# Kernel tuning notes

Hardware: AMD Instinct MI355X
Metric: run time of the kernel (lower is better)

The kernel has to match this reference:

```python
import jax, jax.numpy as jnp
import numpy as np
import math

B, S, D = 8, 1024, 1024
NH, NKV, HD = 16, 8, 64
BLK_NUM, BLK_SIZE = 128, 8

def apply_rope(x, cos, sin):
    # x: (B,S,H,HD); cos/sin: (S, HD//2)
    x1 = x[..., 0::2]
    x2 = x[..., 1::2]
    c = cos[None, :, None, :]
    s = sin[None, :, None, :]
    r1 = x1 * c - x2 * s
    r2 = x1 * s + x2 * c
    out = jnp.stack([r1, r2], axis=-1).reshape(x.shape)
    return out

def setup_inputs() -> dict:
    key = jax.random.key(0)
    ks = jax.random.split(key, 7)
    x = jax.random.normal(ks[0], (B, S, D), dtype=jnp.float32)
    scale = 1.0 / math.sqrt(D)
    wq = jax.random.normal(ks[1], (D, NH * HD), dtype=jnp.float32) * scale
    wk = jax.random.normal(ks[2], (D, NKV * HD), dtype=jnp.float32) * scale
    wv = jax.random.normal(ks[3], (D, NKV * HD), dtype=jnp.float32) * scale
    wo = jax.random.normal(ks[4], (NH * HD, D), dtype=jnp.float32) * scale
    pos = jnp.arange(S, dtype=jnp.float32)
    inv_freq = 1.0 / (10000.0 ** (jnp.arange(0, HD, 2, dtype=jnp.float32) / HD))
    ang = pos[:, None] * inv_freq[None, :]
    freqs_cis_cos = jnp.cos(ang)
    freqs_cis_sin = jnp.sin(ang)
    return {"x": x, "wq": wq, "wk": wk, "wv": wv, "wo": wo,
            "freqs_cis_cos": freqs_cis_cos, "freqs_cis_sin": freqs_cis_sin,
            "start_pos": 0}

def reference(x, wq, wk, wv, wo, freqs_cis_cos, freqs_cis_sin, start_pos):
    q = (x @ wq).reshape(B, S, NH, HD)
    k = (x @ wk).reshape(B, S, NKV, HD)
    v = (x @ wv).reshape(B, S, NKV, HD)
    q = apply_rope(q, freqs_cis_cos, freqs_cis_sin)
    k = apply_rope(k, freqs_cis_cos, freqs_cis_sin)
    # GQA: repeat kv heads
    rep = NH // NKV
    k = jnp.repeat(k, rep, axis=2)  # (B,S,NH,HD)
    v = jnp.repeat(v, rep, axis=2)
    # block-causal mask: q in block i attends to kv blocks j <= i
    blk_id = jnp.arange(S) // BLK_SIZE
    mask = blk_id[:, None] >= blk_id[None, :]  # (S,S)
    scores = jnp.einsum('bqhd,bkhd->bhqk', q, k) / math.sqrt(HD)
    scores = jnp.where(mask[None, None], scores, -jnp.inf)
    attn = jax.nn.softmax(scores, axis=-1)
    out = jnp.einsum('bhqk,bkhd->bqhd', attn, v).reshape(B, S, NH * HD)
    return out @ wo
```

## Files before the change

### kernel.cpp

```cpp
#include <hip/hip_runtime.h>
#include <cstdint>
#include <math.h>

#define B_   8
#define S_   1024
#define D_   1024
#define NH_  16
#define NKV_ 8
#define HD_  64
#define M_   (B_*S_)

using bf16   = __bf16;
using bf16x4 = __attribute__((ext_vector_type(4))) __bf16;
using bf16x8 = __attribute__((ext_vector_type(8))) __bf16;
using f32x4  = __attribute__((ext_vector_type(4))) float;

__device__ __forceinline__ void gll16(const bf16* g, const bf16* l) {
    __builtin_amdgcn_global_load_lds(
        (const __attribute__((address_space(1))) unsigned int*)(uintptr_t)g,
        (__attribute__((address_space(3))) unsigned int*)(uintptr_t)l,
        16, 0, 0);
}

__device__ __forceinline__ void dsr128(bf16x8& d, const bf16* p) {
    asm volatile("ds_read_b128 %0, %1" : "=v"(d) : "v"((unsigned)(uintptr_t)p));
}
__device__ __forceinline__ void lgkm0() {
    asm volatile("s_waitcnt lgkmcnt(0)" ::: "memory");
    __builtin_amdgcn_sched_barrier(0);
}
__device__ __forceinline__ void vm_wait0()  { asm volatile("s_waitcnt vmcnt(0)"  ::: "memory"); }
__device__ __forceinline__ void vm_wait4()  { asm volatile("s_waitcnt vmcnt(4)"  ::: "memory"); }
__device__ __forceinline__ void vm_wait5()  { asm volatile("s_waitcnt vmcnt(5)"  ::: "memory"); }
__device__ __forceinline__ void vm_wait6()  { asm volatile("s_waitcnt vmcnt(6)"  ::: "memory"); }
__device__ __forceinline__ void bar()       { __builtin_amdgcn_s_barrier(); asm volatile("" ::: "memory"); }

__global__ void k_prep1(const float* __restrict__ x,
                        const float* __restrict__ wq, const float* __restrict__ wk,
                        const float* __restrict__ wv, const float* __restrict__ wo,
                        bf16* __restrict__ xb, bf16* __restrict__ wqkvT, bf16* __restrict__ woT) {
    __shared__ float tile[64 * 65];
    int bid = blockIdx.x;
    int t = threadIdx.x;
    if (bid < 8192) {
        int i = bid * 256 + t;
        float4 v = ((const float4*)x)[i];
        bf16x4 o = { (bf16)v.x, (bf16)v.y, (bf16)v.z, (bf16)v.w };
        ((bf16x4*)xb)[i] = o;
        return;
    }
    int b2 = bid - 8192;
    int bx = b2 % 48, by = b2 / 48;
    const int R = 1024;
    const float* in; bf16* out; int C, xo;
    if (bx < 16)      { in = wq; out = wqkvT;               C = 1024; xo = bx; }
    else if (bx < 24) { in = wk; out = wqkvT + 1024 * 1024; C = 512;  xo = bx - 16; }
    else if (bx < 32) { in = wv; out = wqkvT + 1536 * 1024; C = 512;  xo = bx - 24; }
    else              { in = wo; out = woT;                 C = 1024; xo = bx - 32; }
    int r0 = by * 64, c0 = xo * 64;
    #pragma unroll
    for (int it = 0; it < 16; ++it) {
        int idx = it * 256 + t;
        int r = idx >> 6, c = idx & 63;
        tile[r * 65 + c] = in[(size_t)(r0 + r) * C + c0 + c];
    }
    __syncthreads();
    #pragma unroll
    for (int it = 0; it < 16; ++it) {
        int idx = it * 256 + t;
        int c = idx >> 6, r = idx & 63;
        out[(size_t)(c0 + c) * R + r0 + r] = (bf16)tile[r * 65 + c];
    }
}

template <typename OutT, int NI>
__global__ __launch_bounds__(512, 2) void k_gemm8p(const bf16* __restrict__ A,
                                                   const bf16* __restrict__ Bt,
                                                   OutT* __restrict__ C, int M, int N, int K) {
    constexpr int BN = NI * 64;
    __shared__ __align__(16) bf16 aL2[2 * 256 * 64];
    __shared__ __align__(16) bf16 bL2[2 * BN * 64];
    const int t    = threadIdx.x;
    const int lane = t & 63;
    const int w    = t >> 6;
    const int quad = lane >> 4;
    const int l16  = lane & 15;
    const int wr   = w >> 2;
    const int wc   = w & 3;

    int bid = blockIdx.y * gridDim.x + blockIdx.x;
    int cpx = (gridDim.x * gridDim.y) >> 3;
    int sw  = (bid & 7) * cpx + (bid >> 3);
    int bx  = sw % gridDim.x, by = sw / gridDim.x;
    const int m0 = by * 256;
    const int n0 = bx * BN;

    f32x4 acc[8][NI] = {};

    auto stageA2 = [&](int kb, int dbuf, int itX, int itY) {
        const int k0 = kb << 6;
        #pragma unroll
        for (int u = 0; u < 2; ++u) {
            int it = u ? itY : itX;
            int ci = it * 512 + t;
            int r = ci >> 3, c = ci & 7;
            int cg = c ^ (r & 7);
            gll16(A + (size_t)(m0 + r) * K + k0 + cg * 8, aL2 + dbuf * (256 * 64) + ci * 8);
        }
    };
    auto stageBh = [&](int kb, int dbuf, int nh) {
        const int k0 = kb << 6;
        #pragma unroll
        for (int j = 0; j < NI / 2; ++j) {
            int it = nh * (NI / 2) + j;
            int ci = it * 512 + t;
            int lr = ci >> 3, cs = ci & 7;
            int cg = cs ^ (lr & 7);
            int idx = lr - nh * (BN / 2);
            int wcc = idx / (NI * 8);
            int off = idx % (NI * 8);
            int g   = wcc * (NI * 16) + nh * (NI * 8) + off;
            gll16(Bt + (size_t)(n0 + g) * K + k0 + cg * 8, bL2 + dbuf * (BN * 64) + ci * 8);
        }
    };

    auto loadA = [&](const bf16* aL, int mh, bf16x8 (&af)[8]) {
        #pragma unroll
        for (int mi = 0; mi < 4; ++mi)
            #pragma unroll
            for (int kk = 0; kk < 2; ++kk) {
                int row = wr * 128 + (mh * 4 + mi) * 16 + l16;
                int ch  = (kk * 4 + quad) ^ (row & 7);
                dsr128(af[mi * 2 + kk], &aL[row * 64 + ch * 8]);
            }
    };
    auto loadB = [&](const bf16* bL, int nh, bf16x8 (&bfr)[NI]) {
        #pragma unroll
        for (int j = 0; j < NI / 2; ++j)
            #pragma unroll
            for (int kk = 0; kk < 2; ++kk) {
                int lr = nh * (BN / 2) + wc * (NI * 8) + j * 16 + l16;
                int ch = (kk * 4 + quad) ^ (lr & 7);
                dsr128(bfr[j * 2 + kk], &bL[lr * 64 + ch * 8]);
            }
    };
    auto mmac = [&](int mh, int nh, bf16x8 (&af)[8], bf16x8 (&bfr)[NI]) {
        __builtin_amdgcn_s_setprio(1);
        #pragma unroll
        for (int mi = 0; mi < 4; ++mi)
            #pragma unroll
            for (int j = 0; j < NI / 2; ++j)
                #pragma unroll
                for (int kk = 0; kk < 2; ++kk)
                    acc[mh * 4 + mi][nh * (NI / 2) + j] =
                        __builtin_amdgcn_mfma_f32_16x16x32_bf16(af[mi * 2 + kk], bfr[j * 2 + kk],
                                                                acc[mh * 4 + mi][nh * (NI / 2) + j], 0, 0, 0);
        __builtin_amdgcn_s_setprio(0);
    };

    const int NT = K >> 6;

    auto tile = [&](int T, int bufc) {
        const bf16* aL = aL2 + bufc * (256 * 64);
        const bf16* bL = bL2 + bufc * (BN * 64);
        bf16x8 af[8], bfr[NI];
        loadA(aL, 0, af); loadB(bL, 0, bfr);
        if (T + 1 < NT) stageBh(T + 1, bufc ^ 1, 1);
        bar(); lgkm0();
        mmac(0, 0, af, bfr);
        bar();
        loadB(bL, 1, bfr);
        if (T + 2 < NT) stageA2(T + 2, bufc, 0, 2);
        bar(); lgkm0();
        mmac(0, 1, af, bfr);
        bar();
        loadA(aL, 1, af); loadB(bL, 0, bfr);
        bar(); lgkm0();
        mmac(1, 0, af, bfr);
        bar();
        loadB(bL, 1, bfr);
        if (T + 2 < NT) { stageA2(T + 2, bufc, 1, 3); stageBh(T + 2, bufc, 0); }
        bar(); lgkm0();
        mmac(1, 1, af, bfr);
        if (T + 2 < NT) { if constexpr (NI == 4) vm_wait6(); else vm_wait5(); }
        else vm_wait0();
        bar();
    };

    stageA2(0, 0, 0, 2); stageA2(0, 0, 1, 3); stageBh(0, 0, 0); stageBh(0, 0, 1);
    stageA2(1, 1, 0, 2); stageA2(1, 1, 1, 3); stageBh(1, 1, 0);
    if constexpr (NI == 4) vm_wait6(); else vm_wait5();
    bar();

    for (int T = 0; T < NT; T += 2) {
        tile(T, 0);
        tile(T + 1, 1);
    }

    #pragma unroll
    for (int mi = 0; mi < 8; ++mi)
        #pragma unroll
        for (int ni = 0; ni < NI; ++ni)
            #pragma unroll
            for (int r = 0; r < 4; ++r) {
                int row = m0 + wr * 128 + mi * 16 + quad * 4 + r;
                int col = n0 + wc * (NI * 16) + ni * 16 + l16;
                C[(size_t)row * N + col] = (OutT)acc[mi][ni][r];
            }
}

__global__ void k_prep2(const bf16* __restrict__ qkv, const float* __restrict__ cosg,
                        const float* __restrict__ sing, bf16* __restrict__ qd,
                        bf16* __restrict__ kd, bf16* __restrict__ vt) {
    __shared__ __align__(16) bf16 tile[64 * 72];
    int bid = blockIdx.x;
    int t = threadIdx.x;
    if (bid < 8192) {
        if (t < 192) {
            int token = bid;
            int b = token >> 10, s = token & 1023;
            int hh = t >> 3, i8 = t & 7;
            float4 c4 = *(const float4*)&cosg[s * 32 + i8 * 4];
            float4 s4 = *(const float4*)&sing[s * 32 + i8 * 4];
            int srcBase, dstBase;
            bf16* dst;
            float sf;
            if (hh < 16) {
                srcBase = token * 2048 + hh * 64;
                dstBase = ((b * NH_ + hh) * S_ + s) * 64;
                dst = qd;
                sf = 0.180336879f;
            } else {
                int h = hh - 16;
                srcBase = token * 2048 + 1024 + h * 64;
                dstBase = ((b * NKV_ + h) * S_ + s) * 64;
                dst = kd;
                sf = 1.0f;
            }
            bf16x8 v = *(const bf16x8*)&qkv[srcBase + i8 * 8];
            const float cc[4] = { c4.x, c4.y, c4.z, c4.w };
            const float ss[4] = { s4.x, s4.y, s4.z, s4.w };
            bf16x8 o;
            #pragma unroll
            for (int j = 0; j < 4; ++j) {
                float e  = (float)v[2 * j];
                float od = (float)v[2 * j + 1];
                o[2 * j]     = (bf16)(sf * (e * cc[j] - od * ss[j]));
                o[2 * j + 1] = (bf16)(sf * (e * ss[j] + od * cc[j]));
            }
            *(bf16x8*)&dst[dstBase + i8 * 8] = o;
        }
        return;
    }
    int b2 = bid - 8192;
    int st = b2 & 15;
    int h  = (b2 >> 4) & 7;
    int b  = b2 >> 7;
    int s0 = st * 64;
    #pragma unroll
    for (int it = 0; it < 2; ++it) {
        int ci = it * 256 + t;
        int r = ci >> 3, c = ci & 7;
        *(uint4*)&tile[r * 72 + c * 8] =
            *(const uint4*)&qkv[(size_t)(b * S_ + s0 + r) * 2048 + 1536 + h * 64 + c * 8];
    }
    __syncthreads();
    #pragma unroll
    for (int it = 0; it < 2; ++it) {
        int ci = it * 256 + t;
        int d = ci >> 3, sc = ci & 7;
        int g = sc >> 2, q4 = sc & 3;
        bf16x8 v;
        #pragma unroll
        for (int j = 0; j < 8; ++j) {
            int s_ext = g * 32 + q4 * 4 + (j & 3) + 16 * (j >> 2);
            v[j] = tile[s_ext * 72 + d];
        }
        *(bf16x8*)&vt[(size_t)((b * NKV_ + h) * 64 + d) * S_ + s0 + sc * 8] = v;
    }
}

__global__ __launch_bounds__(256, 4) void k_attn(const bf16* __restrict__ q, const bf16* __restrict__ k,
                                                 const bf16* __restrict__ vt, bf16* __restrict__ out) {
    __shared__ __align__(16) bf16 kt[2 * 64 * 64];
    __shared__ __align__(16) bf16 vtt[2 * 64 * 64];
    int bid = blockIdx.x;
    int qt = 15 - (bid >> 7);
    int combo = bid & 127;
    int b = combo >> 4, h = combo & 15;
    int hkv = h >> 1;
    int t = threadIdx.x;
    int w = t >> 6, lane = t & 63, quad = lane >> 4, l16 = lane & 15;

    const bf16* qh = q + (size_t)(b * NH_ + h) * S_ * 64;
    int qw = qt * 64 + w * 16;
    const bf16* qb = qh + (size_t)(qw + l16) * 64;
    bf16x8 qf0 = *(const bf16x8*)(qb + quad * 8);
    bf16x8 qf1 = *(const bf16x8*)(qb + 32 + quad * 8);

    const bf16* kg = k  + (size_t)(b * NKV_ + hkv) * S_ * 64;
    const bf16* vg = vt + (size_t)(b * NKV_ + hkv) * 64 * S_;

    const int sr0 = t >> 3;
    const int cs  = t & 7;

    auto stage = [&](int u, int buf) {
        int k0 = u * 64;
        #pragma unroll
        for (int it = 0; it < 2; ++it) {
            int r  = sr0 + it * 32;
            int cg = cs ^ (r & 7);
            int ci = it * 256 + t;
            gll16(kg + (size_t)(k0 + r) * 64 + cg * 8, kt  + buf * 4096 + ci * 8);
            gll16(vg + (size_t)r * S_ + k0 + cg * 8,   vtt + buf * 4096 + ci * 8);
        }
    };

    const bf16 one = (bf16)1.0f;
    const bf16x8 vones = { one, one, one, one, one, one, one, one };

    f32x4 o[4] = {};
    f32x4 ol = {};
    const int klim = ((qw + l16) & ~7) + 8;

    auto unit = [&](const bf16* ktb, const bf16* vtb, int k0, bool diag) {
        bf16x8 af[8];
        #pragma unroll
        for (int kk = 0; kk < 2; ++kk)
            #pragma unroll
            for (int f = 0; f < 4; ++f) {
                int row = f * 16 + l16;
                int ch  = (kk * 4 + quad) ^ (row & 7);
                dsr128(af[kk * 4 + f], &ktb[row * 64 + ch * 8]);
            }
        lgkm0();
        f32x4 sc[4] = {};
        __builtin_amdgcn_s_setprio(1);
        #pragma unroll
        for (int kk = 0; kk < 2; ++kk)
            #pragma unroll
            for (int f = 0; f < 4; ++f)
                sc[f] = __builtin_amdgcn_mfma_f32_16x16x32_bf16(af[kk * 4 + f], kk ? qf1 : qf0, sc[f], 0, 0, 0);
        __builtin_amdgcn_s_setprio(0);

        bf16x8 vbf[8];
        #pragma unroll
        for (int dc = 0; dc < 4; ++dc)
            #pragma unroll
            for (int kk = 0; kk < 2; ++kk) {
                int row = dc * 16 + l16;
                int ch  = (kk * 4 + quad) ^ (row & 7);
                dsr128(vbf[dc * 2 + kk], &vtb[row * 64 + ch * 8]);
            }

        float p[4][4];
        #pragma unroll
        for (int f = 0; f < 4; ++f)
            #pragma unroll
            for (int r = 0; r < 4; ++r) {
                float pv = __builtin_amdgcn_exp2f(sc[f][r]);
                if (diag && (k0 + f * 16 + quad * 4 + r >= klim)) pv = 0.f;
                p[f][r] = pv;
            }
        bf16x8 pa0, pa1;
        #pragma unroll
        for (int j = 0; j < 4; ++j) {
            pa0[j]     = (bf16)p[0][j];
            pa0[j + 4] = (bf16)p[1][j];
            pa1[j]     = (bf16)p[2][j];
            pa1[j + 4] = (bf16)p[3][j];
        }
        ol = __builtin_amdgcn_mfma_f32_16x16x32_bf16(pa0, vones, ol, 0, 0, 0);
        ol = __builtin_amdgcn_mfma_f32_16x16x32_bf16(pa1, vones, ol, 0, 0, 0);

        lgkm0();
        __builtin_amdgcn_s_setprio(1);
        #pragma unroll
        for (int dc = 0; dc < 4; ++dc)
            #pragma unroll
            for (int kk = 0; kk < 2; ++kk)
                o[dc] = __builtin_amdgcn_mfma_f32_16x16x32_bf16(kk ? pa1 : pa0, vbf[dc * 2 + kk], o[dc], 0, 0, 0);
        __builtin_amdgcn_s_setprio(0);
    };

    const int NU = qt + 1;
    stage(0, 0);
    asm volatile("" :: "v"(qf0), "v"(qf1));

    int u = 0;
    for (; u + 2 <= NU; u += 2) {
        bar();
        stage(u + 1, 1);
        vm_wait4();
        bar();
        unit(kt, vtt, u * 64, false);
        bar();
        bool hn = (u + 2 < NU);
        if (hn) { stage(u + 2, 0); vm_wait4(); } else vm_wait0();
        bar();
        unit(kt + 4096, vtt + 4096, (u + 1) * 64, (u + 1) == NU - 1);
    }
    if (u < NU) {
        bar();
        vm_wait0();
        bar();
        unit(kt, vtt, u * 64, true);
    }

    #pragma unroll
    for (int r = 0; r < 4; ++r) {
        float invl = 1.0f / ol[r];
        #pragma unroll
        for (int dc = 0; dc < 4; ++dc) {
            int row = qw + quad * 4 + r;
            int col = h * 64 + dc * 16 + l16;
            out[(size_t)(b * S_ + row) * 1024 + col] = (bf16)(o[dc][r] * invl);
        }
    }
}

extern "C" void kernel_launch(void* const* d_in, const int* in_sizes, int n_in,
                              void* d_out, int out_size, void* d_ws, size_t ws_size,
                              hipStream_t stream) {
    const float* x  = (const float*)d_in[0];
    const float* wq = (const float*)d_in[1];
    const float* wk = (const float*)d_in[2];
    const float* wv = (const float*)d_in[3];
    const float* wo = (const float*)d_in[4];
    const float* fc = (const float*)d_in[5];
    const float* fs = (const float*)d_in[6];
    (void)in_sizes; (void)n_in; (void)out_size; (void)ws_size;

    char* ws = (char*)d_ws;
    bf16* xb    = (bf16*)(ws);
    bf16* wqkvT = (bf16*)(ws + (16u << 20));
    bf16* woT   = (bf16*)(ws + (20u << 20));
    bf16* qkvb  = (bf16*)(ws + (22u << 20));
    bf16* kb    = (bf16*)(ws + (54u << 20));
    bf16* vtb   = (bf16*)(ws + (62u << 20));
    bf16* qb    = xb;
    bf16* attnb = qkvb;

    k_prep1<<<dim3(8960), dim3(256), 0, stream>>>(x, wq, wk, wv, wo, xb, wqkvT, woT);

    k_gemm8p<bf16, 4><<<dim3(8, 32), dim3(512), 0, stream>>>(xb, wqkvT, qkvb, M_, 2048, 1024);

    k_prep2<<<dim3(9216), dim3(256), 0, stream>>>(qkvb, fc, fs, qb, kb, vtb);

    k_attn<<<dim3(2048), dim3(256), 0, stream>>>(qb, kb, vtb, attnb);

    k_gemm8p<float, 2><<<dim3(8, 32), dim3(512), 0, stream>>>(attnb, woT, (float*)d_out, M_, 1024, 1024);
}
```

Before: 198.8 us.

## Replace 8-wave ping-pong GEMM with 4-wave triple-buffered K=32 GEMM

Both projection GEMMs move from a 512-thread, double-buffered, K=64 kernel with split half-tile MFMA phases and many barriers to a 256-thread kernel. The new kernel uses a 3-stage LDS ring with K=32 slices, one barrier per iteration, and a simpler XOR swizzle. Each wave now computes a larger 128x(NFR*16) tile. The aim is fewer barriers and more loads in flight, at the cost of half as many waves per block, more accumulator registers, and dropping the setprio and explicit ds_read scheduling.

```diff
diff --git a/kernel.cpp b/kernel.cpp
--- a/kernel.cpp
+++ b/kernel.cpp
@@ -31,8 +31,8 @@
 }
 __device__ __forceinline__ void vm_wait0()  { asm volatile("s_waitcnt vmcnt(0)"  ::: "memory"); }
 __device__ __forceinline__ void vm_wait4()  { asm volatile("s_waitcnt vmcnt(4)"  ::: "memory"); }
-__device__ __forceinline__ void vm_wait5()  { asm volatile("s_waitcnt vmcnt(5)"  ::: "memory"); }
 __device__ __forceinline__ void vm_wait6()  { asm volatile("s_waitcnt vmcnt(6)"  ::: "memory"); }
+__device__ __forceinline__ void vm_wait8()  { asm volatile("s_waitcnt vmcnt(8)"  ::: "memory"); }
 __device__ __forceinline__ void bar()       { __builtin_amdgcn_s_barrier(); asm volatile("" ::: "memory"); }
 
 __global__ void k_prep1(const float* __restrict__ x,
@@ -73,20 +73,20 @@
     }
 }
 
-template <typename OutT, int NI>
-__global__ __launch_bounds__(512, 2) void k_gemm8p(const bf16* __restrict__ A,
-                                                   const bf16* __restrict__ Bt,
-                                                   OutT* __restrict__ C, int M, int N, int K) {
-    constexpr int BN = NI * 64;
-    __shared__ __align__(16) bf16 aL2[2 * 256 * 64];
-    __shared__ __align__(16) bf16 bL2[2 * BN * 64];
+template <typename OutT, int NFR>
+__global__ __launch_bounds__(256, 1) void k_gemmW(const bf16* __restrict__ A,
+                                                  const bf16* __restrict__ Bt,
+                                                  OutT* __restrict__ C, int M, int N, int K) {
+    constexpr int BN = NFR * 32;
+    __shared__ __align__(16) bf16 aL3[3 * 256 * 32];
+    __shared__ __align__(16) bf16 bL3[3 * BN * 32];
     const int t    = threadIdx.x;
     const int lane = t & 63;
     const int w    = t >> 6;
     const int quad = lane >> 4;
     const int l16  = lane & 15;
-    const int wr   = w >> 2;
-    const int wc   = w & 3;
+    const int wr   = w >> 1;
+    const int wc   = w & 1;
 
     int bid = blockIdx.y * gridDim.x + blockIdx.x;
     int cpx = (gridDim.x * gridDim.y) >> 3;
@@ -95,116 +95,73 @@
     const int m0 = by * 256;
     const int n0 = bx * BN;
 
-    f32x4 acc[8][NI] = {};
-
-    auto stageA2 = [&](int kb, int dbuf, int itX, int itY) {
-        const int k0 = kb << 6;
-        #pragma unroll
-        for (int u = 0; u < 2; ++u) {
-            int it = u ? itY : itX;
-            int ci = it * 512 + t;
-            int r = ci >> 3, c = ci & 7;
-            int cg = c ^ (r & 7);
-            gll16(A + (size_t)(m0 + r) * K + k0 + cg * 8, aL2 + dbuf * (256 * 64) + ci * 8);
+    f32x4 acc[8][NFR] = {};
+
+    auto stage = [&](int kb, int sb) {
+        const int k0 = kb << 5;
+        #pragma unroll
+        for (int it = 0; it < 4; ++it) {
+            int u = it * 256 + t;
+            int r = u >> 2, c = u & 3;
+            int cg = c ^ ((r & 3) ^ ((r >> 2) & 3));
+            gll16(A + (size_t)(m0 + r) * K + k0 + cg * 8, aL3 + sb * (256 * 32) + u * 8);
+        }
+        #pragma unroll
+        for (int it = 0; it < BN / 64; ++it) {
+            int u = it * 256 + t;
+            int r = u >> 2, c = u & 3;
+            int cg = c ^ ((r & 3) ^ ((r >> 2) & 3));
+            gll16(Bt + (size_t)(n0 + r) * K + k0 + cg * 8, bL3 + sb * (BN * 32) + u * 8);
         }
     };
-    auto stageBh = [&](int kb, int dbuf, int nh) {
-        const int k0 = kb << 6;
-        #pragma unroll
-        for (int j = 0; j < NI / 2; ++j) {
-            int it = nh * (NI / 2) + j;
-            int ci = it * 512 + t;
-            int lr = ci >> 3, cs = ci & 7;
-            int cg = cs ^ (lr & 7);
-            int idx = lr - nh * (BN / 2);
-            int wcc = idx / (NI * 8);
-            int off = idx % (NI * 8);
-            int g   = wcc * (NI * 16) + nh * (NI * 8) + off;
-            gll16(Bt + (size_t)(n0 + g) * K + k0 + cg * 8, bL2 + dbuf * (BN * 64) + ci * 8);
-        }
-    };
-
-    auto loadA = [&](const bf16* aL, int mh, bf16x8 (&af)[8]) {
-        #pragma unroll
-        for (int mi = 0; mi < 4; ++mi)
-            #pragma unroll
-            for (int kk = 0; kk < 2; ++kk) {
-                int row = wr * 128 + (mh * 4 + mi) * 16 + l16;
-                int ch  = (kk * 4 + quad) ^ (row & 7);
-                dsr128(af[mi * 2 + kk], &aL[row * 64 + ch * 8]);
-            }
-    };
-    auto loadB = [&](const bf16* bL, int nh, bf16x8 (&bfr)[NI]) {
-        #pragma unroll
-        for (int j = 0; j < NI / 2; ++j)
-            #pragma unroll
-            for (int kk = 0; kk < 2; ++kk) {
-                int lr = nh * (BN / 2) + wc * (NI * 8) + j * 16 + l16;
-                int ch = (kk * 4 + quad) ^ (lr & 7);
-                dsr128(bfr[j * 2 + kk], &bL[lr * 64 + ch * 8]);
-            }
-    };
-    auto mmac = [&](int mh, int nh, bf16x8 (&af)[8], bf16x8 (&bfr)[NI]) {
-        __builtin_amdgcn_s_setprio(1);
-        #pragma unroll
-        for (int mi = 0; mi < 4; ++mi)
-            #pragma unroll
-            for (int j = 0; j < NI / 2; ++j)
-                #pragma unroll
-                for (int kk = 0; kk < 2; ++kk)
-                    acc[mh * 4 + mi][nh * (NI / 2) + j] =
-                        __builtin_amdgcn_mfma_f32_16x16x32_bf16(af[mi * 2 + kk], bfr[j * 2 + kk],
-                                                                acc[mh * 4 + mi][nh * (NI / 2) + j], 0, 0, 0);
-        __builtin_amdgcn_s_setprio(0);
-    };
-
-    const int NT = K >> 6;
-
-    auto tile = [&](int T, int bufc) {
-        const bf16* aL = aL2 + bufc * (256 * 64);
-        const bf16* bL = bL2 + bufc * (BN * 64);
-        bf16x8 af[8], bfr[NI];
-        loadA(aL, 0, af); loadB(bL, 0, bfr);
-        if (T + 1 < NT) stageBh(T + 1, bufc ^ 1, 1);
-        bar(); lgkm0();
-        mmac(0, 0, af, bfr);
-        bar();
-        loadB(bL, 1, bfr);
-        if (T + 2 < NT) stageA2(T + 2, bufc, 0, 2);
-        bar(); lgkm0();
-        mmac(0, 1, af, bfr);
-        bar();
-        loadA(aL, 1, af); loadB(bL, 0, bfr);
-        bar(); lgkm0();
-        mmac(1, 0, af, bfr);
-        bar();
-        loadB(bL, 1, bfr);
-        if (T + 2 < NT) { stageA2(T + 2, bufc, 1, 3); stageBh(T + 2, bufc, 0); }
-        bar(); lgkm0();
-        mmac(1, 1, af, bfr);
-        if (T + 2 < NT) { if constexpr (NI == 4) vm_wait6(); else vm_wait5(); }
+
+    const int NT = K >> 5;
+
+    stage(0, 0);
+    stage(1, 1);
+
+    int cur = 0;
+    for (int T = 0; T < NT; ++T) {
+        if (T + 1 < NT) { if constexpr (NFR == 8) vm_wait8(); else vm_wait6(); }
         else vm_wait0();
         bar();
-    };
-
-    stageA2(0, 0, 0, 2); stageA2(0, 0, 1, 3); stageBh(0, 0, 0); stageBh(0, 0, 1);
-    stageA2(1, 1, 0, 2); stageA2(1, 1, 1, 3); stageBh(1, 1, 0);
-    if constexpr (NI == 4) vm_wait6(); else vm_wait5();
-    bar();
-
-    for (int T = 0; T < NT; T += 2) {
-        tile(T, 0);
-        tile(T + 1, 1);
+
+        const bf16* aT = aL3 + cur * (256 * 32);
+        const bf16* bT = bL3 + cur * (BN * 32);
+        bf16x8 af[8], bf[NFR];
+        #pragma unroll
+        for (int mi = 0; mi < 8; ++mi) {
+            int row = wr * 128 + mi * 16 + l16;
+            int ch  = quad ^ ((row & 3) ^ ((row >> 2) & 3));
+            af[mi] = *(const bf16x8*)&aT[row * 32 + ch * 8];
+        }
+        #pragma unroll
+        for (int ni = 0; ni < NFR; ++ni) {
+            int row = wc * (NFR * 16) + ni * 16 + l16;
+            int ch  = quad ^ ((row & 3) ^ ((row >> 2) & 3));
+            bf[ni] = *(const bf16x8*)&bT[row * 32 + ch * 8];
+        }
+
+        int stg = cur + 2; if (stg >= 3) stg -= 3;
+        if (T + 2 < NT) stage(T + 2, stg);
+
+        #pragma unroll
+        for (int mi = 0; mi < 8; ++mi)
+            #pragma unroll
+            for (int ni = 0; ni < NFR; ++ni)
+                acc[mi][ni] = __builtin_amdgcn_mfma_f32_16x16x32_bf16(af[mi], bf[ni], acc[mi][ni], 0, 0, 0);
+
+        cur = (cur == 2) ? 0 : cur + 1;
     }
 
     #pragma unroll
     for (int mi = 0; mi < 8; ++mi)
         #pragma unroll
-        for (int ni = 0; ni < NI; ++ni)
+        for (int ni = 0; ni < NFR; ++ni)
             #pragma unroll
             for (int r = 0; r < 4; ++r) {
                 int row = m0 + wr * 128 + mi * 16 + quad * 4 + r;
-                int col = n0 + wc * (NI * 16) + ni * 16 + l16;
+                int col = n0 + wc * (NFR * 16) + ni * 16 + l16;
                 C[(size_t)row * N + col] = (OutT)acc[mi][ni][r];
             }
 }
@@ -443,11 +400,11 @@
 
     k_prep1<<<dim3(8960), dim3(256), 0, stream>>>(x, wq, wk, wv, wo, xb, wqkvT, woT);
 
-    k_gemm8p<bf16, 4><<<dim3(8, 32), dim3(512), 0, stream>>>(xb, wqkvT, qkvb, M_, 2048, 1024);
+    k_gemmW<bf16, 8><<<dim3(8, 32), dim3(256), 0, stream>>>(xb, wqkvT, qkvb, M_, 2048, 1024);
 
     k_prep2<<<dim3(9216), dim3(256), 0, stream>>>(qkvb, fc, fs, qb, kb, vtb);
 
     k_attn<<<dim3(2048), dim3(256), 0, stream>>>(qb, kb, vtb, attnb);
 
-    k_gemm8p<float, 2><<<dim3(8, 32), dim3(512), 0, stream>>>(attnb, woT, (float*)d_out, M_, 1024, 1024);
-}
+    k_gemmW<float, 4><<<dim3(8, 32), dim3(256), 0, stream>>>(attnb, woT, (float*)d_out, M_, 1024, 1024);
+}
```

Measured after the change: 204.6 us. 2.9% more time.
